# Kernel tuning notes

Hardware: AMD Instinct MI355X
Metric: run time of the kernel (lower is better)

The kernel has to match this reference:

```python
import jax, jax.numpy as jnp
import numpy as np


def setup_inputs() -> dict:
    key = jax.random.key(0)
    k1, k2 = jax.random.split(key)
    B, T_enc, T_dec, D = 8, 2048, 2048, 128
    encoder_hidden_states = jax.random.normal(k1, (B, T_enc, D), dtype=jnp.float32)
    decoder_hidden_states = jax.random.normal(k2, (B, T_dec, D), dtype=jnp.float32)
    return {"encoder_hidden_states": encoder_hidden_states,
            "decoder_hidden_states": decoder_hidden_states}


def reference(encoder_hidden_states, decoder_hidden_states):
    # dot_product[b,q,k] = dec[b,q,:] . enc[b,k,:]
    dot_product = jnp.einsum("bqd,bkd->bqk", decoder_hidden_states, encoder_hidden_states)
    # attn_scores[b,q,d] = sum_k dot_product[b,q,k] * enc[b,k,d]
    # (the torch code materializes the 4D broadcast; this is the same math as a bmm)
    attn_scores = jnp.einsum("bqk,bkd->bqd", dot_product, encoder_hidden_states)
    return attn_scores
```

## Files before the change

### kernel.cpp

```cpp
#include <hip/hip_runtime.h>

#define BB 8
#define TT 2048
#define DD 128
#define CH 32
#define GT_STRIDE 72
#define DS_STRIDE 136

typedef __attribute__((ext_vector_type(8))) short bf16x8;
typedef __attribute__((ext_vector_type(4))) float f32x4;
typedef unsigned short u16;

static __device__ __forceinline__ float bf2f(u16 u) {
    union { unsigned int i; float f; } v; v.i = ((unsigned int)u) << 16; return v.f;
}
static __device__ __forceinline__ u16 f2bf(float f) {
    union { float f; unsigned int i; } v; v.f = f;
    unsigned int x = v.i;
    return (u16)((x + 0x7FFFu + ((x >> 16) & 1u)) >> 16);
}

__global__ __launch_bounds__(256, 1) void gram_mfma(const float* __restrict__ enc,
                                                    u16* __restrict__ P) {
    const int b     = blockIdx.y;
    const int chunk = blockIdx.x;
    const int t     = threadIdx.x;

    __shared__ __align__(16) u16 Gt[DD * GT_STRIDE];

    const float* src = enc + ((size_t)b * TT + (size_t)chunk * 64) * DD;
    const int d  = t & 127;
    const int kh = t >> 7;
    #pragma unroll
    for (int a = 0; a < 8; ++a) {
        const int k4 = a * 2 + kh;
        u16 o[4];
        #pragma unroll
        for (int i = 0; i < 4; ++i)
            o[i] = f2bf(src[(k4 * 4 + i) * DD + d]);
        *(ushort4*)&Gt[d * GT_STRIDE + k4 * 4] = *(const ushort4*)o;
    }
    __syncthreads();

    const int wave = t >> 6, lane = t & 63, quad = lane >> 4, ln = lane & 15;

    bf16x8 afrag[2][2];
    #pragma unroll
    for (int mi = 0; mi < 2; ++mi)
        #pragma unroll
        for (int ks = 0; ks < 2; ++ks)
            afrag[mi][ks] = *(const bf16x8*)&Gt[((wave * 2 + mi) * 16 + ln) * GT_STRIDE
                                                + ks * 32 + quad * 8];
    f32x4 acc[2][8];
    #pragma unroll
    for (int mi = 0; mi < 2; ++mi)
        #pragma unroll
        for (int nt = 0; nt < 8; ++nt) acc[mi][nt] = (f32x4){0.f, 0.f, 0.f, 0.f};

    #pragma unroll
    for (int ks = 0; ks < 2; ++ks) {
        #pragma unroll
        for (int nt = 0; nt < 8; ++nt) {
            const bf16x8 bfrag = *(const bf16x8*)&Gt[(nt * 16 + ln) * GT_STRIDE
                                                     + ks * 32 + quad * 8];
            #pragma unroll
            for (int mi = 0; mi < 2; ++mi)
                acc[mi][nt] = __builtin_amdgcn_mfma_f32_16x16x32_bf16(
                    afrag[mi][ks], bfrag, acc[mi][nt], 0, 0, 0);
        }
    }

    u16* Pb = P + ((size_t)chunk * BB + b) * (DD * DD);
    const int off = ln * 16 + (quad >> 1) * 8 + (quad & 1) * 4;
    #pragma unroll
    for (int mi = 0; mi < 2; ++mi) {
        #pragma unroll
        for (int nt = 0; nt < 8; ++nt) {
            u16 o[4];
            #pragma unroll
            for (int r = 0; r < 4; ++r) o[r] = f2bf(acc[mi][nt][r]);
            const int tile = (wave * 2 + mi) * 8 + nt;
            *(ushort4*)&Pb[tile * 256 + off] = *(const ushort4*)o;
        }
    }
}

__global__ __launch_bounds__(256) void gram_reduce(const u16* __restrict__ P,
                                                   u16* __restrict__ Gw) {
    const int g = blockIdx.x * 256 + threadIdx.x;
    const ushort4* Pu = (const ushort4*)P;
    const int stride = BB * DD * DD / 4;
    float sx = 0.f, sy = 0.f, sz = 0.f, sw = 0.f;
    #pragma unroll 8
    for (int c = 0; c < CH; ++c) {
        const ushort4 v = Pu[(size_t)c * stride + g];
        sx += bf2f(v.x); sy += bf2f(v.y); sz += bf2f(v.z); sw += bf2f(v.w);
    }
    ushort4 o; o.x = f2bf(sx); o.y = f2bf(sy); o.z = f2bf(sz); o.w = f2bf(sw);
    ((ushort4*)Gw)[g] = o;
}

__global__ __launch_bounds__(256, 1) void apply_mfma(const float* __restrict__ dec,
                                                     const u16* __restrict__ Gw,
                                                     float* __restrict__ out) {
    const int b     = blockIdx.y;
    const int chunk = blockIdx.x;
    const int t     = threadIdx.x;

    __shared__ __align__(16) u16 Gs[DD * DD];
    __shared__ __align__(16) u16 Ds[64 * DS_STRIDE];

    const uint4* gsrc = (const uint4*)(Gw + (size_t)b * DD * DD);
    #pragma unroll
    for (int i = 0; i < 8; ++i)
        ((uint4*)Gs)[i * 256 + t] = gsrc[i * 256 + t];

    const float4* dsrc = (const float4*)(dec + ((size_t)b * TT + (size_t)chunk * 64) * DD);
    #pragma unroll
    for (int i = 0; i < 8; ++i) {
        const int idx = i * 256 + t;
        const int row = idx >> 5, c4 = idx & 31;
        const float4 v = dsrc[idx];
        u16 o[4] = {f2bf(v.x), f2bf(v.y), f2bf(v.z), f2bf(v.w)};
        *(ushort4*)&Ds[row * DS_STRIDE + c4 * 4] = *(const ushort4*)o;
    }
    __syncthreads();

    const int wave = t >> 6, lane = t & 63, quad = lane >> 4, ln = lane & 15;
    const int qt = wave * 16;

    f32x4 acc[8];
    #pragma unroll
    for (int dt = 0; dt < 8; ++dt) acc[dt] = (f32x4){0.f, 0.f, 0.f, 0.f};

    #pragma unroll
    for (int ks = 0; ks < 4; ++ks) {
        const bf16x8 a = *(const bf16x8*)&Ds[(qt + ln) * DS_STRIDE + ks * 32 + quad * 8];
        const int mtk  = ks * 2 + (quad >> 1);
        const int boff = ln * 16 + (quad & 1) * 8;
        #pragma unroll
        for (int dt = 0; dt < 8; ++dt) {
            const bf16x8 bb = *(const bf16x8*)&Gs[(mtk * 8 + dt) * 256 + boff];
            acc[dt] = __builtin_amdgcn_mfma_f32_16x16x32_bf16(a, bb, acc[dt], 0, 0, 0);
        }
    }

    float* ob = out + ((size_t)b * TT + (size_t)chunk * 64) * DD;
    #pragma unroll
    for (int dt = 0; dt < 8; ++dt) {
        const int dcol = dt * 16 + ln;
        #pragma unroll
        for (int r = 0; r < 4; ++r) {
            const int q = qt + quad * 4 + r;
            ob[q * DD + dcol] = acc[dt][r];
        }
    }
}

extern "C" void kernel_launch(void* const* d_in, const int* in_sizes, int n_in,
                              void* d_out, int out_size, void* d_ws, size_t ws_size,
                              hipStream_t stream) {
    const float* enc = (const float*)d_in[0];
    const float* dec = (const float*)d_in[1];
    float* out = (float*)d_out;

    u16* P  = (u16*)d_ws;
    u16* Gw = (u16*)((char*)d_ws + (size_t)CH * BB * DD * DD * sizeof(u16));

    gram_mfma<<<dim3(CH, BB), 256, 0, stream>>>(enc, P);
    gram_reduce<<<BB * DD * DD / 4 / 256, 256, 0, stream>>>(P, Gw);
    apply_mfma<<<dim3(TT / 64, BB), 256, 0, stream>>>(dec, Gw, out);
}
```

Measured before the change: 76.66 us.

## Fuse Gram partial reduction into apply kernel and cut chunk count to 8

Each gram block now loops over four 64-row tiles, so there are 8 partial Gram matrices per batch instead of 32. The separate reduce kernel is dropped: every apply block sums the 8 bf16 partials for its batch directly into shared memory. This removes one launch and the global round trip of the reduced matrix. In exchange each of the 256 apply blocks redundantly reads 8 partials, and the gram stage runs only 64 blocks, which is low parallelism.

```diff
diff --git a/kernel.cpp b/kernel.cpp
--- a/kernel.cpp
+++ b/kernel.cpp
@@ -3,7 +3,7 @@
 #define BB 8
 #define TT 2048
 #define DD 128
-#define CH 32
+#define CH 8
 #define GT_STRIDE 72
 #define DS_STRIDE 136
 
@@ -28,45 +28,48 @@
 
     __shared__ __align__(16) u16 Gt[DD * GT_STRIDE];
 
-    const float* src = enc + ((size_t)b * TT + (size_t)chunk * 64) * DD;
     const int d  = t & 127;
     const int kh = t >> 7;
-    #pragma unroll
-    for (int a = 0; a < 8; ++a) {
-        const int k4 = a * 2 + kh;
-        u16 o[4];
-        #pragma unroll
-        for (int i = 0; i < 4; ++i)
-            o[i] = f2bf(src[(k4 * 4 + i) * DD + d]);
-        *(ushort4*)&Gt[d * GT_STRIDE + k4 * 4] = *(const ushort4*)o;
-    }
-    __syncthreads();
-
     const int wave = t >> 6, lane = t & 63, quad = lane >> 4, ln = lane & 15;
 
-    bf16x8 afrag[2][2];
-    #pragma unroll
-    for (int mi = 0; mi < 2; ++mi)
-        #pragma unroll
-        for (int ks = 0; ks < 2; ++ks)
-            afrag[mi][ks] = *(const bf16x8*)&Gt[((wave * 2 + mi) * 16 + ln) * GT_STRIDE
-                                                + ks * 32 + quad * 8];
     f32x4 acc[2][8];
     #pragma unroll
     for (int mi = 0; mi < 2; ++mi)
         #pragma unroll
         for (int nt = 0; nt < 8; ++nt) acc[mi][nt] = (f32x4){0.f, 0.f, 0.f, 0.f};
 
-    #pragma unroll
-    for (int ks = 0; ks < 2; ++ks) {
+    for (int tt = 0; tt < 4; ++tt) {
+        const float* src = enc + ((size_t)b * TT + (size_t)chunk * 256 + tt * 64) * DD;
+        if (tt) __syncthreads();
         #pragma unroll
-        for (int nt = 0; nt < 8; ++nt) {
-            const bf16x8 bfrag = *(const bf16x8*)&Gt[(nt * 16 + ln) * GT_STRIDE
-                                                     + ks * 32 + quad * 8];
+        for (int a = 0; a < 8; ++a) {
+            const int k4 = a * 2 + kh;
+            u16 o[4];
             #pragma unroll
-            for (int mi = 0; mi < 2; ++mi)
-                acc[mi][nt] = __builtin_amdgcn_mfma_f32_16x16x32_bf16(
-                    afrag[mi][ks], bfrag, acc[mi][nt], 0, 0, 0);
+            for (int i = 0; i < 4; ++i)
+                o[i] = f2bf(src[(k4 * 4 + i) * DD + d]);
+            *(ushort4*)&Gt[d * GT_STRIDE + k4 * 4] = *(const ushort4*)o;
+        }
+        __syncthreads();
+
+        bf16x8 afrag[2][2];
+        #pragma unroll
+        for (int mi = 0; mi < 2; ++mi)
+            #pragma unroll
+            for (int ks = 0; ks < 2; ++ks)
+                afrag[mi][ks] = *(const bf16x8*)&Gt[((wave * 2 + mi) * 16 + ln) * GT_STRIDE
+                                                    + ks * 32 + quad * 8];
+        #pragma unroll
+        for (int ks = 0; ks < 2; ++ks) {
+            #pragma unroll
+            for (int nt = 0; nt < 8; ++nt) {
+                const bf16x8 bfrag = *(const bf16x8*)&Gt[(nt * 16 + ln) * GT_STRIDE
+                                                         + ks * 32 + quad * 8];
+                #pragma unroll
+                for (int mi = 0; mi < 2; ++mi)
+                    acc[mi][nt] = __builtin_amdgcn_mfma_f32_16x16x32_bf16(
+                        afrag[mi][ks], bfrag, acc[mi][nt], 0, 0, 0);
+            }
         }
     }
 
@@ -85,23 +88,8 @@
     }
 }
 
-__global__ __launch_bounds__(256) void gram_reduce(const u16* __restrict__ P,
-                                                   u16* __restrict__ Gw) {
-    const int g = blockIdx.x * 256 + threadIdx.x;
-    const ushort4* Pu = (const ushort4*)P;
-    const int stride = BB * DD * DD / 4;
-    float sx = 0.f, sy = 0.f, sz = 0.f, sw = 0.f;
-    #pragma unroll 8
-    for (int c = 0; c < CH; ++c) {
-        const ushort4 v = Pu[(size_t)c * stride + g];
-        sx += bf2f(v.x); sy += bf2f(v.y); sz += bf2f(v.z); sw += bf2f(v.w);
-    }
-    ushort4 o; o.x = f2bf(sx); o.y = f2bf(sy); o.z = f2bf(sz); o.w = f2bf(sw);
-    ((ushort4*)Gw)[g] = o;
-}
-
 __global__ __launch_bounds__(256, 1) void apply_mfma(const float* __restrict__ dec,
-                                                     const u16* __restrict__ Gw,
+                                                     const u16* __restrict__ P,
                                                      float* __restrict__ out) {
     const int b     = blockIdx.y;
     const int chunk = blockIdx.x;
@@ -110,10 +98,23 @@
     __shared__ __align__(16) u16 Gs[DD * DD];
     __shared__ __align__(16) u16 Ds[64 * DS_STRIDE];
 
-    const uint4* gsrc = (const uint4*)(Gw + (size_t)b * DD * DD);
-    #pragma unroll
-    for (int i = 0; i < 8; ++i)
-        ((uint4*)Gs)[i * 256 + t] = gsrc[i * 256 + t];
+    {
+        const ushort4* Pu = (const ushort4*)P;
+        const int cstride = BB * DD * DD / 4;
+        const int bbase   = b * (DD * DD / 4);
+        #pragma unroll 4
+        for (int i = 0; i < 16; ++i) {
+            const int g = i * 256 + t;
+            float sx = 0.f, sy = 0.f, sz = 0.f, sw = 0.f;
+            #pragma unroll
+            for (int c = 0; c < CH; ++c) {
+                const ushort4 v = Pu[(size_t)c * cstride + bbase + g];
+                sx += bf2f(v.x); sy += bf2f(v.y); sz += bf2f(v.z); sw += bf2f(v.w);
+            }
+            u16 o[4] = {f2bf(sx), f2bf(sy), f2bf(sz), f2bf(sw)};
+            *(ushort4*)&Gs[g * 4] = *(const ushort4*)o;
+        }
+    }
 
     const float4* dsrc = (const float4*)(dec + ((size_t)b * TT + (size_t)chunk * 64) * DD);
     #pragma unroll
@@ -164,10 +165,8 @@
     const float* dec = (const float*)d_in[1];
     float* out = (float*)d_out;
 
-    u16* P  = (u16*)d_ws;
-    u16* Gw = (u16*)((char*)d_ws + (size_t)CH * BB * DD * DD * sizeof(u16));
+    u16* P = (u16*)d_ws;
 
     gram_mfma<<<dim3(CH, BB), 256, 0, stream>>>(enc, P);
-    gram_reduce<<<BB * DD * DD / 4 / 256, 256, 0, stream>>>(P, Gw);
-    apply_mfma<<<dim3(TT / 64, BB), 256, 0, stream>>>(dec, Gw, out);
+    apply_mfma<<<dim3(TT / 64, BB), 256, 0, stream>>>(dec, P, out);
 }
```

Measured after the change: 88.18 us. 1.15x slower.
